# Performance work log

Hardware: AMD Instinct MI355X
Metric: run time of the kernel (lower is better)

## Reference

```python
import jax, jax.numpy as jnp
import numpy as np

MARGIN = 0.3


def setup_inputs() -> dict:
    key = jax.random.key(0)
    k1, k2 = jax.random.split(key)
    inputs = jax.random.normal(k1, (8192, 1024), dtype=jnp.float32)
    targets = jax.random.randint(k2, (8192,), 0, 128, dtype=jnp.int64)
    return {"inputs": inputs, "targets": targets}


def reference(inputs, targets):
    n = inputs.shape[0] // 2
    rgb = inputs[:n]          # [n, d]
    ir = inputs[n:]           # [n, d]
    # dist[i, j] = || rgb_i - ir_j ||_2
    sq = (jnp.sum(rgb * rgb, axis=1)[:, None]
          + jnp.sum(ir * ir, axis=1)[None, :]
          - 2.0 * (rgb @ ir.T))
    dist = jnp.sqrt(jnp.clip(sq, 1e-12))
    # mask[i, j] = (targets_rgb[j] == targets_ir[i])  -- faithful to
    # targets[:n].expand(n,n).eq(targets[n:].expand(n,n).t())
    mask = targets[None, :n] == targets[n:, None]     # [n, n] bool
    inf = jnp.inf
    # RGB side: per-row hardest positive / easiest negative
    rgb_ap = jnp.max(jnp.where(mask, dist, -inf), axis=1)
    rgb_an = jnp.min(jnp.where(mask, inf, dist), axis=1)
    # IR side: per-column hardest positive / easiest negative
    ir_ap = jnp.max(jnp.where(mask, dist, -inf), axis=0)
    ir_an = jnp.min(jnp.where(mask, inf, dist), axis=0)
    # MarginRankingLoss(an, ap, y=1) = mean(relu(margin - (an - ap)))
    loss = (jnp.mean(jax.nn.relu(MARGIN - (rgb_an - rgb_ap)))
            + jnp.mean(jax.nn.relu(MARGIN - (ir_an - ir_ap))))
    return loss
```

## Files before the change

### kernel.cpp

```cpp
#include <hip/hip_runtime.h>

#define MARGIN 0.3f
#define INF_BITS 0x7f800000
#define NINF_BITS 0xff800000

typedef __attribute__((ext_vector_type(8))) short bf16x8;
typedef __attribute__((ext_vector_type(4))) float f32x4;

__device__ inline unsigned short f2bf(float x) {
    unsigned int u = __float_as_uint(x);
    unsigned int r = (u + 0x7fffu + ((u >> 16) & 1u)) >> 16;
    return (unsigned short)r;
}

__device__ __forceinline__ void gload16(const unsigned short* g, char* l) {
    __builtin_amdgcn_global_load_lds(
        (const __attribute__((address_space(1))) void*)g,
        (__attribute__((address_space(3))) void*)l, 16, 0, 0);
}

__device__ __forceinline__ void stage_half(const unsigned short* g, char* l) {
    gload16(g, l);
    gload16(g + 65536, l + 8192);
}

__global__ void __launch_bounds__(256) prep_kernel(
    const float* __restrict__ in, unsigned short* __restrict__ bf,
    float* __restrict__ norms, int* __restrict__ red)
{
    const int wid = threadIdx.x >> 6, lane = threadIdx.x & 63;
    const int row = blockIdx.x * 4 + wid;
    const size_t base = (size_t)row * 1024;
    float s = 0.f;
    #pragma unroll
    for (int k = 0; k < 4; ++k) {
        const float4 v = ((const float4*)(in + base))[lane + 64 * k];
        s += v.x * v.x + v.y * v.y + v.z * v.z + v.w * v.w;
        ushort4 o;
        o.x = f2bf(v.x); o.y = f2bf(v.y); o.z = f2bf(v.z); o.w = f2bf(v.w);
        ((ushort4*)(bf + base))[lane + 64 * k] = o;
    }
    #pragma unroll
    for (int off = 32; off > 0; off >>= 1) s += __shfl_down(s, off);
    if (lane == 0) norms[row] = s;
    if (blockIdx.x < 64) {
        int i = blockIdx.x * 256 + threadIdx.x;
        red[i] = ((i >> 12) & 1) ? INF_BITS : 0;
    }
}

#define VM_WAIT(n) asm volatile("s_waitcnt vmcnt(" #n ")" ::: "memory")

#define STAGE_A(h, kt, b) \
    stage_half(pA + (h)*131072 + (((kt) & 15) << 6), lds + (b)*65536 + (h)*16384 + tid*16)
#define STAGE_B(h, kt, b) \
    stage_half(pB + (h)*131072 + (((kt) & 15) << 6), lds + (b)*65536 + 32768 + (h)*16384 + tid*16)

#define PHASE(qq, bc, STAGE_STMT, WAIT_STMT)                                     \
  {                                                                              \
    const char* ab = lds + (bc) * 65536 + aoff + (2 * (qq)) * 2048;              \
    bf16x8 a0k0 = *(const bf16x8*)(ab + swz0);                                   \
    bf16x8 a0k1 = *(const bf16x8*)(ab + swz1);                                   \
    bf16x8 a1k0 = *(const bf16x8*)(ab + 2048 + swz0);                            \
    bf16x8 a1k1 = *(const bf16x8*)(ab + 2048 + swz1);                            \
    if ((qq) == 0) {                                                             \
      const char* bb = lds + (bc) * 65536 + boff;                                \
      _Pragma("unroll")                                                          \
      for (int n = 0; n < 4; ++n) {                                              \
        bk0[n] = *(const bf16x8*)(bb + n * 2048 + swz0);                         \
        bk1[n] = *(const bf16x8*)(bb + n * 2048 + swz1);                         \
      }                                                                          \
    }                                                                            \
    STAGE_STMT;                                                                  \
    if ((qq) == 0) asm volatile("s_waitcnt lgkmcnt(8)" ::: "memory");            \
    __builtin_amdgcn_s_barrier();                                                \
    asm volatile("s_waitcnt lgkmcnt(0)" ::: "memory");                           \
    __builtin_amdgcn_sched_barrier(0);                                           \
    __builtin_amdgcn_s_setprio(1);                                               \
    _Pragma("unroll")                                                            \
    for (int n = 0; n < 4; ++n) {                                                \
      acc[2*(qq)][n]   = __builtin_amdgcn_mfma_f32_16x16x32_bf16(a0k0, bk0[n], acc[2*(qq)][n], 0, 0, 0);   \
      acc[2*(qq)+1][n] = __builtin_amdgcn_mfma_f32_16x16x32_bf16(a1k0, bk0[n], acc[2*(qq)+1][n], 0, 0, 0); \
    }                                                                            \
    _Pragma("unroll")                                                            \
    for (int n = 0; n < 4; ++n) {                                                \
      acc[2*(qq)][n]   = __builtin_amdgcn_mfma_f32_16x16x32_bf16(a0k1, bk1[n], acc[2*(qq)][n], 0, 0, 0);   \
      acc[2*(qq)+1][n] = __builtin_amdgcn_mfma_f32_16x16x32_bf16(a1k1, bk1[n], acc[2*(qq)+1][n], 0, 0, 0); \
    }                                                                            \
    __builtin_amdgcn_s_setprio(0);                                               \
    WAIT_STMT;                                                                   \
    __builtin_amdgcn_s_barrier();                                                \
  }

__global__ void __launch_bounds__(512, 2) dist_kernel(
    const unsigned short* __restrict__ Abf, const unsigned short* __restrict__ Bbf,
    const float* __restrict__ na, const float* __restrict__ nb,
    const int* __restrict__ tgt,
    int* __restrict__ g_rgb_ap, int* __restrict__ g_rgb_an,
    int* __restrict__ g_ir_ap, int* __restrict__ g_ir_an)
{
    extern __shared__ char lds[];

    const int tid  = threadIdx.x;
    const int lane = tid & 63;
    const int wid  = tid >> 6;
    const int wr   = wid >> 2;
    const int wc   = wid & 3;
    const int l4 = lane >> 4, rsel = lane & 15;

    const int lin = blockIdx.y * 16 + blockIdx.x;
    const int xcd = lin & 7, idx = lin >> 3;
    const int brow = (xcd >> 1) * 4 + (idx >> 3);
    const int bcol = (xcd & 1) * 8 + (idx & 7);

    const int r0 = tid >> 3;
    const int cs = (tid & 7) << 4;
    const int c0 = (cs ^ ((r0 & 7) << 4)) >> 1;
    const unsigned short* pA = Abf + (size_t)(brow * 256 + r0) * 1024 + c0;
    const unsigned short* pB = Bbf + (size_t)(bcol * 256 + r0) * 1024 + c0;

    const int swz0 = ((l4 ^ (rsel & 7)) << 4);
    const int swz1 = (((4 + l4) ^ (rsel & 7)) << 4);
    const int aoff = wr * 16384 + rsel * 128;
    const int boff = 32768 + (wc >> 1) * 16384 + (wc & 1) * 8192 + rsel * 128;

    f32x4 acc[8][4];
    const f32x4 zero = {0.f, 0.f, 0.f, 0.f};
    #pragma unroll
    for (int m = 0; m < 8; ++m)
        #pragma unroll
        for (int n = 0; n < 4; ++n)
            acc[m][n] = zero;

    bf16x8 bk0[4], bk1[4];

    STAGE_A(0, 0, 0); STAGE_A(1, 0, 0);
    STAGE_B(0, 0, 0); STAGE_B(1, 0, 0);
    STAGE_B(0, 1, 1); STAGE_B(1, 1, 1);
    VM_WAIT(4);
    __builtin_amdgcn_s_barrier();

    for (int i = 0; i < 8; ++i) {
        const int t = 2 * i;
        PHASE(0, 0, STAGE_A(0, t + 1, 1), );
        PHASE(1, 0, STAGE_A(1, t + 1, 1), );
        PHASE(2, 0, STAGE_B(0, t + 2, 0), );
        PHASE(3, 0, STAGE_B(1, t + 2, 0), VM_WAIT(4));
        PHASE(0, 1, STAGE_A(0, t + 2, 0), );
        PHASE(1, 1, STAGE_A(1, t + 2, 0), );
        PHASE(2, 1, STAGE_B(0, t + 3, 1), );
        PHASE(3, 1, STAGE_B(1, t + 3, 1), VM_WAIT(4));
    }

    VM_WAIT(0);
    __syncthreads();

    char* rowbase = lds;
    float* colMax = (float*)(lds + 135168);
    float* colMin = (float*)(lds + 144384);

    const float NINF = __int_as_float((int)NINF_BITS);
    const float PINF = __int_as_float(INF_BITS);

    int jg[4], ltc[4];
    float nbv[4];
    #pragma unroll
    for (int n = 0; n < 4; ++n) {
        jg[n] = bcol * 256 + wc * 64 + n * 16 + rsel;
        ltc[n] = tgt[jg[n]];
        nbv[n] = nb[jg[n]];
    }

    float cmax[4] = {NINF, NINF, NINF, NINF};
    float cmin[4] = {PINF, PINF, PINF, PINF};

    #pragma unroll
    for (int m = 0; m < 8; ++m) {
        #pragma unroll
        for (int r = 0; r < 4; ++r) {
            const int lrow = wr * 128 + m * 16 + l4 * 4 + r;
            const int ig = brow * 256 + lrow;
            const int lt = tgt[4096 + ig];
            const float nav = na[ig];
            float rx = NINF, rn = PINF;
            #pragma unroll
            for (int n = 0; n < 4; ++n) {
                const float urow = __builtin_fmaf(-2.0f, acc[m][n][r], nbv[n]);
                const float ucol = __builtin_fmaf(-2.0f, acc[m][n][r], nav);
                const bool match = (ltc[n] == lt);
                rx = match ? fmaxf(rx, urow) : rx;
                rn = match ? rn : fminf(rn, urow);
                cmax[n] = match ? fmaxf(cmax[n], ucol) : cmax[n];
                cmin[n] = match ? cmin[n] : fminf(cmin[n], ucol);
            }
            float2* rp = (float2*)(rowbase + lrow * 528 + (wc * 16 + rsel) * 8);
            *rp = make_float2(rx, rn);
        }
    }
    #pragma unroll
    for (int n = 0; n < 4; ++n) {
        const int lcol = wc * 64 + n * 16 + rsel;
        colMax[lcol * 9 + wr * 4 + l4] = cmax[n];
        colMin[lcol * 9 + wr * 4 + l4] = cmin[n];
    }
    __syncthreads();

    if (tid < 256) {
        const int row = tid;
        const f32x4* rp = (const f32x4*)(rowbase + row * 528);
        float rmax = NINF, rmin = PINF;
        #pragma unroll 8
        for (int s = 0; s < 32; ++s) {
            const f32x4 v = rp[s];
            rmax = fmaxf(rmax, fmaxf(v[0], v[2]));
            rmin = fminf(rmin, fminf(v[1], v[3]));
        }
        const int ig = brow * 256 + row;
        const float nav = na[ig];
        const float ap = sqrtf(fmaxf(nav + rmax, 1e-12f));
        const float an = sqrtf(fmaxf(nav + rmin, 1e-12f));
        atomicMax(&g_rgb_ap[ig], __float_as_int(ap));
        atomicMin(&g_rgb_an[ig], __float_as_int(an));
    } else {
        const int col = tid & 255;
        float cm = NINF, cn = PINF;
        #pragma unroll
        for (int s = 0; s < 8; ++s) {
            cm = fmaxf(cm, colMax[col * 9 + s]);
            cn = fminf(cn, colMin[col * 9 + s]);
        }
        const int jgc = bcol * 256 + col;
        const float nbc = nb[jgc];
        const float ap = sqrtf(fmaxf(nbc + cm, 1e-12f));
        const float an = sqrtf(fmaxf(nbc + cn, 1e-12f));
        atomicMax(&g_ir_ap[jgc], __float_as_int(ap));
        atomicMin(&g_ir_an[jgc], __float_as_int(an));
    }
}

__global__ void __launch_bounds__(256) loss_kernel(
    const int* __restrict__ red, float* __restrict__ out)
{
    float s = 0.f;
    const int t = threadIdx.x;
    #pragma unroll
    for (int k = 0; k < 4; ++k) {
        const int idx = k * 256 + t;
        const int4 ap  = ((const int4*)(red))[idx];
        const int4 an  = ((const int4*)(red + 4096))[idx];
        const int4 ap2 = ((const int4*)(red + 8192))[idx];
        const int4 an2 = ((const int4*)(red + 12288))[idx];
        s += fmaxf(0.f, MARGIN - (__int_as_float(an.x) - __int_as_float(ap.x)));
        s += fmaxf(0.f, MARGIN - (__int_as_float(an.y) - __int_as_float(ap.y)));
        s += fmaxf(0.f, MARGIN - (__int_as_float(an.z) - __int_as_float(ap.z)));
        s += fmaxf(0.f, MARGIN - (__int_as_float(an.w) - __int_as_float(ap.w)));
        s += fmaxf(0.f, MARGIN - (__int_as_float(an2.x) - __int_as_float(ap2.x)));
        s += fmaxf(0.f, MARGIN - (__int_as_float(an2.y) - __int_as_float(ap2.y)));
        s += fmaxf(0.f, MARGIN - (__int_as_float(an2.z) - __int_as_float(ap2.z)));
        s += fmaxf(0.f, MARGIN - (__int_as_float(an2.w) - __int_as_float(ap2.w)));
    }
    #pragma unroll
    for (int off = 32; off > 0; off >>= 1) s += __shfl_down(s, off);
    __shared__ float wsum[4];
    if ((threadIdx.x & 63) == 0) wsum[threadIdx.x >> 6] = s;
    __syncthreads();
    if (threadIdx.x == 0) out[0] = (wsum[0] + wsum[1] + wsum[2] + wsum[3]) / 4096.0f;
}

extern "C" void kernel_launch(void* const* d_in, const int* in_sizes, int n_in,
                              void* d_out, int out_size, void* d_ws, size_t ws_size,
                              hipStream_t stream) {
    (void)in_sizes; (void)n_in; (void)out_size; (void)ws_size;
    const float* input = (const float*)d_in[0];
    const int* tgt = (const int*)d_in[1];
    float* out = (float*)d_out;

    unsigned short* bf = (unsigned short*)d_ws;
    float* norms = (float*)(bf + (size_t)8192 * 1024);
    int* red = (int*)(norms + 8192);

    hipFuncSetAttribute((const void*)dist_kernel,
                        hipFuncAttributeMaxDynamicSharedMemorySize, 153600);

    prep_kernel<<<2048, 256, 0, stream>>>(input, bf, norms, red);
    dist_kernel<<<dim3(16, 16), 512, 153600, stream>>>(
        bf, bf + (size_t)4096 * 1024, norms, norms + 4096, tgt,
        red, red + 4096, red + 8192, red + 12288);
    loss_kernel<<<1, 256, 0, stream>>>(red, out);
}
```

Measured before the change: 47.53 us.

## Fuse bf16 conversion and norm computation into distance GEMM load pipeline

Removes the separate prep kernel. The distance kernel now loads fp32 inputs directly into registers, converts them to bf16 with packed convert instructions, writes them to LDS, and accumulates squared norms along the way. Norms are then reduced through LDS instead of being read from global memory. This drops the bf16 round-trip through global memory and one launch. In exchange, each tile reads twice as many bytes from global memory, A/B tiles are re-read by many blocks, staging now goes through registers instead of direct-to-LDS loads, and norms are computed from fp32 per block.

```diff
diff --git a/kernel.cpp b/kernel.cpp
--- a/kernel.cpp
+++ b/kernel.cpp
@@ -7,56 +7,42 @@
 typedef __attribute__((ext_vector_type(8))) short bf16x8;
 typedef __attribute__((ext_vector_type(4))) float f32x4;
 
-__device__ inline unsigned short f2bf(float x) {
-    unsigned int u = __float_as_uint(x);
-    unsigned int r = (u + 0x7fffu + ((u >> 16) & 1u)) >> 16;
-    return (unsigned short)r;
-}
-
-__device__ __forceinline__ void gload16(const unsigned short* g, char* l) {
-    __builtin_amdgcn_global_load_lds(
-        (const __attribute__((address_space(1))) void*)g,
-        (__attribute__((address_space(3))) void*)l, 16, 0, 0);
-}
-
-__device__ __forceinline__ void stage_half(const unsigned short* g, char* l) {
-    gload16(g, l);
-    gload16(g + 65536, l + 8192);
-}
-
-__global__ void __launch_bounds__(256) prep_kernel(
-    const float* __restrict__ in, unsigned short* __restrict__ bf,
-    float* __restrict__ norms, int* __restrict__ red)
-{
-    const int wid = threadIdx.x >> 6, lane = threadIdx.x & 63;
-    const int row = blockIdx.x * 4 + wid;
-    const size_t base = (size_t)row * 1024;
-    float s = 0.f;
-    #pragma unroll
-    for (int k = 0; k < 4; ++k) {
-        const float4 v = ((const float4*)(in + base))[lane + 64 * k];
-        s += v.x * v.x + v.y * v.y + v.z * v.z + v.w * v.w;
-        ushort4 o;
-        o.x = f2bf(v.x); o.y = f2bf(v.y); o.z = f2bf(v.z); o.w = f2bf(v.w);
-        ((ushort4*)(bf + base))[lane + 64 * k] = o;
-    }
-    #pragma unroll
-    for (int off = 32; off > 0; off >>= 1) s += __shfl_down(s, off);
-    if (lane == 0) norms[row] = s;
-    if (blockIdx.x < 64) {
-        int i = blockIdx.x * 256 + threadIdx.x;
-        red[i] = ((i >> 12) & 1) ? INF_BITS : 0;
-    }
-}
-
-#define VM_WAIT(n) asm volatile("s_waitcnt vmcnt(" #n ")" ::: "memory")
-
-#define STAGE_A(h, kt, b) \
-    stage_half(pA + (h)*131072 + (((kt) & 15) << 6), lds + (b)*65536 + (h)*16384 + tid*16)
-#define STAGE_B(h, kt, b) \
-    stage_half(pB + (h)*131072 + (((kt) & 15) << 6), lds + (b)*65536 + 32768 + (h)*16384 + tid*16)
-
-#define PHASE(qq, bc, STAGE_STMT, WAIT_STMT)                                     \
+__device__ __forceinline__ unsigned int cvtpk(float lo, float hi) {
+    unsigned int r;
+    asm("v_cvt_pk_bf16_f32 %0, %1, %2" : "=v"(r) : "v"(lo), "v"(hi));
+    return r;
+}
+
+__global__ void __launch_bounds__(256) init_kernel(int* __restrict__ red) {
+    int i = blockIdx.x * 256 + threadIdx.x;
+    red[i] = ((i >> 12) & 1) ? INF_BITS : 0;
+}
+
+
+#define ISSUE(set, P, eoff) {                                  \
+    stg[set][0] = *(const float4*)((P) + (eoff));              \
+    stg[set][1] = *(const float4*)((P) + (eoff) + 4);          \
+    stg[set][2] = *(const float4*)((P) + (eoff) + 65536);      \
+    stg[set][3] = *(const float4*)((P) + (eoff) + 65536 + 4); }
+
+#define SQ8(v0, v1) ((v0).x*(v0).x + (v0).y*(v0).y + (v0).z*(v0).z + (v0).w*(v0).w + \
+                     (v1).x*(v1).x + (v1).y*(v1).y + (v1).z*(v1).z + (v1).w*(v1).w)
+
+#define WRITE(set, off, NARR, i0, i1) {                                       \
+    unsigned int w0 = cvtpk(stg[set][0].x, stg[set][0].y);                    \
+    unsigned int w1 = cvtpk(stg[set][0].z, stg[set][0].w);                    \
+    unsigned int w2 = cvtpk(stg[set][1].x, stg[set][1].y);                    \
+    unsigned int w3 = cvtpk(stg[set][1].z, stg[set][1].w);                    \
+    unsigned int w4 = cvtpk(stg[set][2].x, stg[set][2].y);                    \
+    unsigned int w5 = cvtpk(stg[set][2].z, stg[set][2].w);                    \
+    unsigned int w6 = cvtpk(stg[set][3].x, stg[set][3].y);                    \
+    unsigned int w7 = cvtpk(stg[set][3].z, stg[set][3].w);                    \
+    *(uint4*)(lds + (off) + tid * 16)        = make_uint4(w0, w1, w2, w3);    \
+    *(uint4*)(lds + (off) + 8192 + tid * 16) = make_uint4(w4, w5, w6, w7);    \
+    NARR[i0] += SQ8(stg[set][0], stg[set][1]);                                \
+    NARR[i1] += SQ8(stg[set][2], stg[set][3]); }
+
+#define PHASE(qq, bc, WRITE_STMT, ISSUE_STMT)                                    \
   {                                                                              \
     const char* ab = lds + (bc) * 65536 + aoff + (2 * (qq)) * 2048;              \
     bf16x8 a0k0 = *(const bf16x8*)(ab + swz0);                                   \
@@ -71,8 +57,8 @@
         bk1[n] = *(const bf16x8*)(bb + n * 2048 + swz1);                         \
       }                                                                          \
     }                                                                            \
-    STAGE_STMT;                                                                  \
-    if ((qq) == 0) asm volatile("s_waitcnt lgkmcnt(8)" ::: "memory");            \
+    WRITE_STMT;                                                                  \
+    ISSUE_STMT;                                                                  \
     __builtin_amdgcn_s_barrier();                                                \
     asm volatile("s_waitcnt lgkmcnt(0)" ::: "memory");                           \
     __builtin_amdgcn_sched_barrier(0);                                           \
@@ -88,13 +74,11 @@
       acc[2*(qq)+1][n] = __builtin_amdgcn_mfma_f32_16x16x32_bf16(a1k1, bk1[n], acc[2*(qq)+1][n], 0, 0, 0); \
     }                                                                            \
     __builtin_amdgcn_s_setprio(0);                                               \
-    WAIT_STMT;                                                                   \
     __builtin_amdgcn_s_barrier();                                                \
   }
 
 __global__ void __launch_bounds__(512, 2) dist_kernel(
-    const unsigned short* __restrict__ Abf, const unsigned short* __restrict__ Bbf,
-    const float* __restrict__ na, const float* __restrict__ nb,
+    const float* __restrict__ Afp, const float* __restrict__ Bfp,
     const int* __restrict__ tgt,
     int* __restrict__ g_rgb_ap, int* __restrict__ g_rgb_an,
     int* __restrict__ g_ir_ap, int* __restrict__ g_ir_an)
@@ -114,10 +98,9 @@
     const int bcol = (xcd & 1) * 8 + (idx & 7);
 
     const int r0 = tid >> 3;
-    const int cs = (tid & 7) << 4;
-    const int c0 = (cs ^ ((r0 & 7) << 4)) >> 1;
-    const unsigned short* pA = Abf + (size_t)(brow * 256 + r0) * 1024 + c0;
-    const unsigned short* pB = Bbf + (size_t)(bcol * 256 + r0) * 1024 + c0;
+    const int c0 = (((tid & 7) ^ (r0 & 7)) << 3);
+    const float* pAf = Afp + (size_t)(brow * 256 + r0) * 1024 + c0;
+    const float* pBf = Bfp + (size_t)(bcol * 256 + r0) * 1024 + c0;
 
     const int swz0 = ((l4 ^ (rsel & 7)) << 4);
     const int swz1 = (((4 + l4) ^ (rsel & 7)) << 4);
@@ -133,26 +116,76 @@
             acc[m][n] = zero;
 
     bf16x8 bk0[4], bk1[4];
-
-    STAGE_A(0, 0, 0); STAGE_A(1, 0, 0);
-    STAGE_B(0, 0, 0); STAGE_B(1, 0, 0);
-    STAGE_B(0, 1, 1); STAGE_B(1, 1, 1);
-    VM_WAIT(4);
+    float4 stg[2][4];
+    float nA[4] = {0.f, 0.f, 0.f, 0.f};
+    float nB[4] = {0.f, 0.f, 0.f, 0.f};
+
+    ISSUE(0, pAf, 0);
+    ISSUE(1, pAf, 131072);
+    WRITE(0, 0,      nA, 0, 1); ISSUE(0, pBf, 0);
+    WRITE(1, 16384,  nA, 2, 3); ISSUE(1, pBf, 131072);
+    WRITE(0, 32768,  nB, 0, 1); ISSUE(0, pBf, 64);
+    WRITE(1, 49152,  nB, 2, 3); ISSUE(1, pBf, 131072 + 64);
+    WRITE(0, 98304,  nB, 0, 1);
+    WRITE(1, 114688, nB, 2, 3);
+    asm volatile("s_waitcnt lgkmcnt(0)" ::: "memory");
     __builtin_amdgcn_s_barrier();
 
-    for (int i = 0; i < 8; ++i) {
-        const int t = 2 * i;
-        PHASE(0, 0, STAGE_A(0, t + 1, 1), );
-        PHASE(1, 0, STAGE_A(1, t + 1, 1), );
-        PHASE(2, 0, STAGE_B(0, t + 2, 0), );
-        PHASE(3, 0, STAGE_B(1, t + 2, 0), VM_WAIT(4));
-        PHASE(0, 1, STAGE_A(0, t + 2, 0), );
-        PHASE(1, 1, STAGE_A(1, t + 2, 0), );
-        PHASE(2, 1, STAGE_B(0, t + 3, 1), );
-        PHASE(3, 1, STAGE_B(1, t + 3, 1), VM_WAIT(4));
-    }
-
-    VM_WAIT(0);
+    PHASE(0, 0, ,                          ISSUE(0, pAf, 64));
+    PHASE(1, 0, ,                          ISSUE(1, pAf, 131072 + 64));
+    PHASE(2, 0, WRITE(0, 65536,  nA, 0, 1), ISSUE(0, pBf, 128));
+    PHASE(3, 0, WRITE(1, 81920,  nA, 2, 3), ISSUE(1, pBf, 131072 + 128));
+    PHASE(0, 1, WRITE(0, 32768,  nB, 0, 1), ISSUE(0, pAf, 128));
+    PHASE(1, 1, WRITE(1, 49152,  nB, 2, 3), ISSUE(1, pAf, 131072 + 128));
+    PHASE(2, 1, WRITE(0, 0,      nA, 0, 1), ISSUE(0, pBf, 192));
+    PHASE(3, 1, WRITE(1, 16384,  nA, 2, 3), ISSUE(1, pBf, 131072 + 192));
+
+    for (int i = 1; i < 7; ++i) {
+        const int t64 = 2 * i * 64;
+        PHASE(0, 0, WRITE(0, 98304,  nB, 0, 1), ISSUE(0, pAf, t64 + 64));
+        PHASE(1, 0, WRITE(1, 114688, nB, 2, 3), ISSUE(1, pAf, 131072 + t64 + 64));
+        PHASE(2, 0, WRITE(0, 65536,  nA, 0, 1), ISSUE(0, pBf, t64 + 128));
+        PHASE(3, 0, WRITE(1, 81920,  nA, 2, 3), ISSUE(1, pBf, 131072 + t64 + 128));
+        PHASE(0, 1, WRITE(0, 32768,  nB, 0, 1), ISSUE(0, pAf, t64 + 128));
+        PHASE(1, 1, WRITE(1, 49152,  nB, 2, 3), ISSUE(1, pAf, 131072 + t64 + 128));
+        PHASE(2, 1, WRITE(0, 0,      nA, 0, 1), ISSUE(0, pBf, t64 + 192));
+        PHASE(3, 1, WRITE(1, 16384,  nA, 2, 3), ISSUE(1, pBf, 131072 + t64 + 192));
+    }
+
+    PHASE(0, 0, WRITE(0, 98304,  nB, 0, 1), ISSUE(0, pAf, 960));
+    PHASE(1, 0, WRITE(1, 114688, nB, 2, 3), ISSUE(1, pAf, 131072 + 960));
+    PHASE(2, 0, WRITE(0, 65536,  nA, 0, 1), );
+    PHASE(3, 0, WRITE(1, 81920,  nA, 2, 3), );
+    PHASE(0, 1, , );
+    PHASE(1, 1, , );
+    PHASE(2, 1, , );
+    PHASE(3, 1, , );
+
+    __syncthreads();
+
+    float* normA = (float*)lds;
+    float* normB = (float*)(lds + 8192);
+    const int slot = tid & 7;
+    normA[(r0      ) * 8 + slot] = nA[0];
+    normA[(r0 +  64) * 8 + slot] = nA[1];
+    normA[(r0 + 128) * 8 + slot] = nA[2];
+    normA[(r0 + 192) * 8 + slot] = nA[3];
+    normB[(r0      ) * 8 + slot] = nB[0];
+    normB[(r0 +  64) * 8 + slot] = nB[1];
+    normB[(r0 + 128) * 8 + slot] = nB[2];
+    normB[(r0 + 192) * 8 + slot] = nB[3];
+    __syncthreads();
+
+    float* na_s = (float*)(lds + 153600);
+    float* nb_s = (float*)(lds + 154624);
+    {
+        const int rr = tid & 255;
+        const float* src = (tid < 256) ? normA : normB;
+        float s = 0.f;
+        #pragma unroll
+        for (int q = 0; q < 8; ++q) s += src[rr * 8 + q];
+        ((tid < 256) ? na_s : nb_s)[rr] = s;
+    }
     __syncthreads();
 
     char* rowbase = lds;
@@ -166,9 +199,10 @@
     float nbv[4];
     #pragma unroll
     for (int n = 0; n < 4; ++n) {
-        jg[n] = bcol * 256 + wc * 64 + n * 16 + rsel;
+        const int lc = wc * 64 + n * 16 + rsel;
+        jg[n] = bcol * 256 + lc;
         ltc[n] = tgt[jg[n]];
-        nbv[n] = nb[jg[n]];
+        nbv[n] = nb_s[lc];
     }
 
     float cmax[4] = {NINF, NINF, NINF, NINF};
@@ -181,7 +215,7 @@
             const int lrow = wr * 128 + m * 16 + l4 * 4 + r;
             const int ig = brow * 256 + lrow;
             const int lt = tgt[4096 + ig];
-            const float nav = na[ig];
+            const float nav = na_s[lrow];
             float rx = NINF, rn = PINF;
             #pragma unroll
             for (int n = 0; n < 4; ++n) {
@@ -216,7 +250,7 @@
             rmin = fminf(rmin, fminf(v[1], v[3]));
         }
         const int ig = brow * 256 + row;
-        const float nav = na[ig];
+        const float nav = na_s[row];
         const float ap = sqrtf(fmaxf(nav + rmax, 1e-12f));
         const float an = sqrtf(fmaxf(nav + rmin, 1e-12f));
         atomicMax(&g_rgb_ap[ig], __float_as_int(ap));
@@ -230,7 +264,7 @@
             cn = fminf(cn, colMin[col * 9 + s]);
         }
         const int jgc = bcol * 256 + col;
-        const float nbc = nb[jgc];
+        const float nbc = nb_s[col];
         const float ap = sqrtf(fmaxf(nbc + cm, 1e-12f));
         const float an = sqrtf(fmaxf(nbc + cn, 1e-12f));
         atomicMax(&g_ir_ap[jgc], __float_as_int(ap));
@@ -275,16 +309,14 @@
     const int* tgt = (const int*)d_in[1];
     float* out = (float*)d_out;
 
-    unsigned short* bf = (unsigned short*)d_ws;
-    float* norms = (float*)(bf + (size_t)8192 * 1024);
-    int* red = (int*)(norms + 8192);
+    int* red = (int*)d_ws;
 
     hipFuncSetAttribute((const void*)dist_kernel,
-                        hipFuncAttributeMaxDynamicSharedMemorySize, 153600);
-
-    prep_kernel<<<2048, 256, 0, stream>>>(input, bf, norms, red);
-    dist_kernel<<<dim3(16, 16), 512, 153600, stream>>>(
-        bf, bf + (size_t)4096 * 1024, norms, norms + 4096, tgt,
+                        hipFuncAttributeMaxDynamicSharedMemorySize, 155648);
+
+    init_kernel<<<64, 256, 0, stream>>>(red);
+    dist_kernel<<<dim3(16, 16), 512, 155648, stream>>>(
+        input, input + (size_t)4096 * 1024, tgt,
         red, red + 4096, red + 8192, red + 12288);
     loss_kernel<<<1, 256, 0, stream>>>(red, out);
 }
```

New measurement: 120.8 us. 2.54x slower.

## Double-buffer B fragments in registers and peel final K iteration

Applied to the files above, without the earlier changes.

B-operand fragments for the next LDS buffer are now prefetched into a second register set, spread across phases 1-3 of the current buffer. The first phase of each buffer therefore no longer stalls on a burst of B loads. The last K iteration is peeled so no out-of-range tiles are staged, which removes the wrap-around masking and the redundant loads. This uses more VGPRs for the extra fragment set and changes the vmcnt wait points, which could hurt occupancy or leave a correctness race if the waits are wrong.

```diff
diff --git a/kernel.cpp b/kernel.cpp
--- a/kernel.cpp
+++ b/kernel.cpp
@@ -52,40 +52,44 @@
 #define VM_WAIT(n) asm volatile("s_waitcnt vmcnt(" #n ")" ::: "memory")
 
 #define STAGE_A(h, kt, b) \
-    stage_half(pA + (h)*131072 + (((kt) & 15) << 6), lds + (b)*65536 + (h)*16384 + tid*16)
+    stage_half(pA + (h)*131072 + ((kt) << 6), lds + (b)*65536 + (h)*16384 + tid*16)
 #define STAGE_B(h, kt, b) \
-    stage_half(pB + (h)*131072 + (((kt) & 15) << 6), lds + (b)*65536 + 32768 + (h)*16384 + tid*16)
-
-#define PHASE(qq, bc, STAGE_STMT, WAIT_STMT)                                     \
+    stage_half(pB + (h)*131072 + ((kt) << 6), lds + (b)*65536 + 32768 + (h)*16384 + tid*16)
+
+#define EB1(B0, B1, SB) \
+    B0[0] = *(const bf16x8*)((SB) + swz0); \
+    B1[0] = *(const bf16x8*)((SB) + swz1); \
+    B0[1] = *(const bf16x8*)((SB) + 2048 + swz0);
+#define EB2(B0, B1, SB) \
+    B1[1] = *(const bf16x8*)((SB) + 2048 + swz1); \
+    B0[2] = *(const bf16x8*)((SB) + 4096 + swz0); \
+    B1[2] = *(const bf16x8*)((SB) + 4096 + swz1);
+#define EB3(B0, B1, SB) \
+    B0[3] = *(const bf16x8*)((SB) + 6144 + swz0); \
+    B1[3] = *(const bf16x8*)((SB) + 6144 + swz1);
+
+#define PHASE(qq, bc, BK0, BK1, EXTRA, STAGE_STMT, WAIT_STMT)                    \
   {                                                                              \
     const char* ab = lds + (bc) * 65536 + aoff + (2 * (qq)) * 2048;              \
     bf16x8 a0k0 = *(const bf16x8*)(ab + swz0);                                   \
     bf16x8 a0k1 = *(const bf16x8*)(ab + swz1);                                   \
     bf16x8 a1k0 = *(const bf16x8*)(ab + 2048 + swz0);                            \
     bf16x8 a1k1 = *(const bf16x8*)(ab + 2048 + swz1);                            \
-    if ((qq) == 0) {                                                             \
-      const char* bb = lds + (bc) * 65536 + boff;                                \
-      _Pragma("unroll")                                                          \
-      for (int n = 0; n < 4; ++n) {                                              \
-        bk0[n] = *(const bf16x8*)(bb + n * 2048 + swz0);                         \
-        bk1[n] = *(const bf16x8*)(bb + n * 2048 + swz1);                         \
-      }                                                                          \
-    }                                                                            \
+    EXTRA                                                                        \
     STAGE_STMT;                                                                  \
-    if ((qq) == 0) asm volatile("s_waitcnt lgkmcnt(8)" ::: "memory");            \
     __builtin_amdgcn_s_barrier();                                                \
     asm volatile("s_waitcnt lgkmcnt(0)" ::: "memory");                           \
     __builtin_amdgcn_sched_barrier(0);                                           \
     __builtin_amdgcn_s_setprio(1);                                               \
     _Pragma("unroll")                                                            \
     for (int n = 0; n < 4; ++n) {                                                \
-      acc[2*(qq)][n]   = __builtin_amdgcn_mfma_f32_16x16x32_bf16(a0k0, bk0[n], acc[2*(qq)][n], 0, 0, 0);   \
-      acc[2*(qq)+1][n] = __builtin_amdgcn_mfma_f32_16x16x32_bf16(a1k0, bk0[n], acc[2*(qq)+1][n], 0, 0, 0); \
+      acc[2*(qq)][n]   = __builtin_amdgcn_mfma_f32_16x16x32_bf16(a0k0, BK0[n], acc[2*(qq)][n], 0, 0, 0);   \
+      acc[2*(qq)+1][n] = __builtin_amdgcn_mfma_f32_16x16x32_bf16(a1k0, BK0[n], acc[2*(qq)+1][n], 0, 0, 0); \
     }                                                                            \
     _Pragma("unroll")                                                            \
     for (int n = 0; n < 4; ++n) {                                                \
-      acc[2*(qq)][n]   = __builtin_amdgcn_mfma_f32_16x16x32_bf16(a0k1, bk1[n], acc[2*(qq)][n], 0, 0, 0);   \
-      acc[2*(qq)+1][n] = __builtin_amdgcn_mfma_f32_16x16x32_bf16(a1k1, bk1[n], acc[2*(qq)+1][n], 0, 0, 0); \
+      acc[2*(qq)][n]   = __builtin_amdgcn_mfma_f32_16x16x32_bf16(a0k1, BK1[n], acc[2*(qq)][n], 0, 0, 0);   \
+      acc[2*(qq)+1][n] = __builtin_amdgcn_mfma_f32_16x16x32_bf16(a1k1, BK1[n], acc[2*(qq)+1][n], 0, 0, 0); \
     }                                                                            \
     __builtin_amdgcn_s_setprio(0);                                               \
     WAIT_STMT;                                                                   \
@@ -123,6 +127,8 @@
     const int swz1 = (((4 + l4) ^ (rsel & 7)) << 4);
     const int aoff = wr * 16384 + rsel * 128;
     const int boff = 32768 + (wc >> 1) * 16384 + (wc & 1) * 8192 + rsel * 128;
+    const char* bB0 = lds + boff;
+    const char* bB1 = lds + 65536 + boff;
 
     f32x4 acc[8][4];
     const f32x4 zero = {0.f, 0.f, 0.f, 0.f};
@@ -132,7 +138,7 @@
         for (int n = 0; n < 4; ++n)
             acc[m][n] = zero;
 
-    bf16x8 bk0[4], bk1[4];
+    bf16x8 bkA0[4], bkA1[4], bkB0[4], bkB1[4];
 
     STAGE_A(0, 0, 0); STAGE_A(1, 0, 0);
     STAGE_B(0, 0, 0); STAGE_B(1, 0, 0);
@@ -140,19 +146,33 @@
     VM_WAIT(4);
     __builtin_amdgcn_s_barrier();
 
-    for (int i = 0; i < 8; ++i) {
+    #pragma unroll
+    for (int n = 0; n < 4; ++n) {
+        bkA0[n] = *(const bf16x8*)(bB0 + n * 2048 + swz0);
+        bkA1[n] = *(const bf16x8*)(bB0 + n * 2048 + swz1);
+    }
+
+    for (int i = 0; i < 7; ++i) {
         const int t = 2 * i;
-        PHASE(0, 0, STAGE_A(0, t + 1, 1), );
-        PHASE(1, 0, STAGE_A(1, t + 1, 1), );
-        PHASE(2, 0, STAGE_B(0, t + 2, 0), );
-        PHASE(3, 0, STAGE_B(1, t + 2, 0), VM_WAIT(4));
-        PHASE(0, 1, STAGE_A(0, t + 2, 0), );
-        PHASE(1, 1, STAGE_A(1, t + 2, 0), );
-        PHASE(2, 1, STAGE_B(0, t + 3, 1), );
-        PHASE(3, 1, STAGE_B(1, t + 3, 1), VM_WAIT(4));
-    }
-
-    VM_WAIT(0);
+        PHASE(0, 0, bkA0, bkA1, , STAGE_A(0, t + 1, 1), VM_WAIT(2));
+        PHASE(1, 0, bkA0, bkA1, EB1(bkB0, bkB1, bB1), STAGE_A(1, t + 1, 1), );
+        PHASE(2, 0, bkA0, bkA1, EB2(bkB0, bkB1, bB1), STAGE_B(0, t + 2, 0), );
+        PHASE(3, 0, bkA0, bkA1, EB3(bkB0, bkB1, bB1), STAGE_B(1, t + 2, 0), VM_WAIT(4));
+        PHASE(0, 1, bkB0, bkB1, , STAGE_A(0, t + 2, 0), VM_WAIT(2));
+        PHASE(1, 1, bkB0, bkB1, EB1(bkA0, bkA1, bB0), STAGE_A(1, t + 2, 0), );
+        PHASE(2, 1, bkB0, bkB1, EB2(bkA0, bkA1, bB0), STAGE_B(0, t + 3, 1), );
+        PHASE(3, 1, bkB0, bkB1, EB3(bkA0, bkA1, bB0), STAGE_B(1, t + 3, 1), VM_WAIT(4));
+    }
+
+    PHASE(0, 0, bkA0, bkA1, , STAGE_A(0, 15, 1), VM_WAIT(2));
+    PHASE(1, 0, bkA0, bkA1, EB1(bkB0, bkB1, bB1), STAGE_A(1, 15, 1), );
+    PHASE(2, 0, bkA0, bkA1, EB2(bkB0, bkB1, bB1), , );
+    PHASE(3, 0, bkA0, bkA1, EB3(bkB0, bkB1, bB1), , VM_WAIT(0));
+    PHASE(0, 1, bkB0, bkB1, , , );
+    PHASE(1, 1, bkB0, bkB1, , , );
+    PHASE(2, 1, bkB0, bkB1, , , );
+    PHASE(3, 1, bkB0, bkB1, , , );
+
     __syncthreads();
 
     char* rowbase = lds;
```

Measured after the change: 47.00 us. Within noise of the previous version (-1.1%).
